# Kernel tuning notes

Hardware: AMD Instinct MI355X
Metric: run time of the kernel (lower is better)

The kernel has to match this reference:

```python
import jax, jax.numpy as jnp
import numpy as np

B, T, D = 4, 2048, 768
H = 12
DH = D // H
DFF = 3072
EPS = 1e-5


def _layernorm(x, g, b):
    mu = jnp.mean(x, axis=-1, keepdims=True)
    var = jnp.var(x, axis=-1, keepdims=True)
    return (x - mu) * jax.lax.rsqrt(var + EPS) * g + b


def setup_inputs() -> dict:
    key = jax.random.key(0)
    ks = jax.random.split(key, 12)
    s = lambda fan_in: 1.0 / np.sqrt(fan_in)
    return {
        "x": jax.random.normal(ks[0], (B, T, D), dtype=jnp.float32),
        "ln1_g": jnp.ones((D,), jnp.float32),
        "ln1_b": jnp.zeros((D,), jnp.float32),
        "w_qkv": jax.random.uniform(ks[1], (D, 3 * D), jnp.float32, -s(D), s(D)),
        "b_qkv": jax.random.uniform(ks[2], (3 * D,), jnp.float32, -s(D), s(D)),
        "w_proj": jax.random.uniform(ks[3], (D, D), jnp.float32, -s(D), s(D)),
        "b_proj": jax.random.uniform(ks[4], (D,), jnp.float32, -s(D), s(D)),
        "ln2_g": jnp.ones((D,), jnp.float32),
        "ln2_b": jnp.zeros((D,), jnp.float32),
        "w_ff1": jax.random.uniform(ks[5], (D, DFF), jnp.float32, -s(D), s(D)),
        "b_ff1": jax.random.uniform(ks[6], (DFF,), jnp.float32, -s(D), s(D)),
        "w_ff2": jax.random.uniform(ks[7], (DFF, D), jnp.float32, -s(DFF), s(DFF)),
        "b_ff2": jax.random.uniform(ks[8], (D,), jnp.float32, -s(DFF), s(DFF)),
    }


def reference(x, ln1_g, ln1_b, w_qkv, b_qkv, w_proj, b_proj,
              ln2_g, ln2_b, w_ff1, b_ff1, w_ff2, b_ff2):
    # --- attention sublayer ---
    h = _layernorm(x, ln1_g, ln1_b)
    qkv = h @ w_qkv + b_qkv                       # [B,T,3D]
    q, k, v = jnp.split(qkv, 3, axis=-1)
    q = q.reshape(B, T, H, DH).transpose(0, 2, 1, 3)  # [B,H,T,DH]
    k = k.reshape(B, T, H, DH).transpose(0, 2, 1, 3)
    v = v.reshape(B, T, H, DH).transpose(0, 2, 1, 3)
    att = jnp.einsum('bhqd,bhkd->bhqk', q, k) / jnp.sqrt(jnp.float32(DH))
    causal = jnp.tril(jnp.ones((T, T), dtype=bool))
    att = jnp.where(causal, att, -jnp.inf)
    att = jax.nn.softmax(att, axis=-1)
    out = jnp.einsum('bhqk,bhkd->bhqd', att, v)    # [B,H,T,DH]
    out = out.transpose(0, 2, 1, 3).reshape(B, T, D)
    x = x + out @ w_proj + b_proj
    # --- MLP sublayer ---
    h2 = _layernorm(x, ln2_g, ln2_b)
    h2 = jax.nn.gelu(h2 @ w_ff1 + b_ff1, approximate=False)
    x = x + h2 @ w_ff2 + b_ff2
    return x
```

## Files before the change

### kernel.cpp

```cpp
#include <hip/hip_runtime.h>
#include <cstdint>
#include <cstddef>

typedef unsigned short u16;
typedef unsigned int u32;
typedef __attribute__((ext_vector_type(8))) short s16x8;
typedef __attribute__((ext_vector_type(4))) float f32x4;

#define NB 4
#define NT 2048
#define ND 768
#define NH 12
#define NDH 64
#define NFF 3072
#define NM (NB*NT)

__device__ __forceinline__ u16 f2b(float f){
  union { float f; unsigned u; } c; c.f = f;
  unsigned r = c.u + 0x7fffu + ((c.u >> 16) & 1u);
  return (u16)(r >> 16);
}

__device__ __forceinline__ f32x4 mfma16(s16x8 a, s16x8 b, f32x4 c){
  return __builtin_amdgcn_mfma_f32_16x16x32_bf16(a, b, c, 0, 0, 0);
}

__device__ __forceinline__ void stage16(u16* lds, const u16* g){
  __builtin_amdgcn_global_load_lds(
      (const __attribute__((address_space(1))) unsigned int*)g,
      (__attribute__((address_space(3))) unsigned int*)lds,
      16, 0, 0);
}

__global__ __launch_bounds__(256) void transpose_bf16(
    const float* __restrict__ in, u16* __restrict__ out, int K, int N)
{
  __shared__ float tile[32][33];
  const int n0 = blockIdx.x * 32, k0 = blockIdx.y * 32;
  const int tx = threadIdx.x, ty = threadIdx.y;
  #pragma unroll
  for (int i = 0; i < 32; i += 8)
    tile[ty + i][tx] = in[(size_t)(k0 + ty + i) * N + n0 + tx];
  __syncthreads();
  #pragma unroll
  for (int i = 0; i < 32; i += 8)
    out[(size_t)(n0 + ty + i) * K + k0 + tx] = f2b(tile[tx][ty + i]);
}

__global__ __launch_bounds__(256) void ln_kernel(
    const float* __restrict__ x, const float* __restrict__ g,
    const float* __restrict__ b, u16* __restrict__ out)
{
  const int row = blockIdx.x;
  const int t = threadIdx.x;
  const float* xr = x + (size_t)row * ND;
  float v0 = xr[t], v1 = xr[t + 256], v2 = xr[t + 512];
  float s = v0 + v1 + v2;
  float ss = v0*v0 + v1*v1 + v2*v2;
  #pragma unroll
  for (int o = 32; o; o >>= 1) { s += __shfl_xor(s, o, 64); ss += __shfl_xor(ss, o, 64); }
  __shared__ float red[8];
  const int w = t >> 6;
  if ((t & 63) == 0) { red[w] = s; red[4 + w] = ss; }
  __syncthreads();
  s  = red[0] + red[1] + red[2] + red[3];
  ss = red[4] + red[5] + red[6] + red[7];
  const float mu = s * (1.f / ND);
  const float var = ss * (1.f / ND) - mu * mu;
  const float rinv = rsqrtf(var + 1e-5f);
  u16* orow = out + (size_t)row * ND;
  orow[t]       = f2b((v0 - mu) * rinv * g[t]       + b[t]);
  orow[t + 256] = f2b((v1 - mu) * rinv * g[t + 256] + b[t + 256]);
  orow[t + 512] = f2b((v2 - mu) * rinv * g[t + 512] + b[t + 512]);
}

template<int EPI>
__global__ __launch_bounds__(256,4) void gemm_bt(
    const u16* __restrict__ A, const u16* __restrict__ Bt,
    const float* __restrict__ bias, const float* __restrict__ res,
    void* __restrict__ o0, void* __restrict__ o1, void* __restrict__ o2,
    const int M, const int N, const int K)
{
  __shared__ u16 As[2][128 * 32];
  __shared__ u16 Bs[2][128 * 32];
  const int tid = threadIdx.x;
  const int lane = tid & 63, wid = tid >> 6;
  const int wr = wid >> 1, wc = wid & 1;
  const int lg = lane >> 4, lm = lane & 15;
  const int bm = blockIdx.x * 128, bn = blockIdx.y * 128;

  f32x4 acc[4][4] = {};

  const u16* ApT = A  + (size_t)(bm + (tid >> 2)) * K + (tid & 3) * 8;
  const u16* BpT = Bt + (size_t)(bn + (tid >> 2)) * K + (tid & 3) * 8;
  const size_t rs64 = (size_t)64 * K;
  const int woff = wid * 512;

  stage16(&As[0][woff],        ApT);
  stage16(&As[0][woff + 2048], ApT + rs64);
  stage16(&Bs[0][woff],        BpT);
  stage16(&Bs[0][woff + 2048], BpT + rs64);
  __syncthreads();

  int cur = 0;
  const int nt = K >> 5;
  for (int t = 1; t < nt; ++t) {
    const int k0 = t << 5;
    stage16(&As[cur ^ 1][woff],        ApT + k0);
    stage16(&As[cur ^ 1][woff + 2048], ApT + rs64 + k0);
    stage16(&Bs[cur ^ 1][woff],        BpT + k0);
    stage16(&Bs[cur ^ 1][woff + 2048], BpT + rs64 + k0);
    s16x8 af[4], bf[4];
    #pragma unroll
    for (int i = 0; i < 4; i++) af[i] = *(const s16x8*)&As[cur][(wr * 64 + i * 16 + lm) * 32 + lg * 8];
    #pragma unroll
    for (int j = 0; j < 4; j++) bf[j] = *(const s16x8*)&Bs[cur][(wc * 64 + j * 16 + lm) * 32 + lg * 8];
    #pragma unroll
    for (int i = 0; i < 4; i++)
      #pragma unroll
      for (int j = 0; j < 4; j++)
        acc[i][j] = mfma16(af[i], bf[j], acc[i][j]);
    __syncthreads();
    cur ^= 1;
  }
  {
    s16x8 af[4], bf[4];
    #pragma unroll
    for (int i = 0; i < 4; i++) af[i] = *(const s16x8*)&As[cur][(wr * 64 + i * 16 + lm) * 32 + lg * 8];
    #pragma unroll
    for (int j = 0; j < 4; j++) bf[j] = *(const s16x8*)&Bs[cur][(wc * 64 + j * 16 + lm) * 32 + lg * 8];
    #pragma unroll
    for (int i = 0; i < 4; i++)
      #pragma unroll
      for (int j = 0; j < 4; j++)
        acc[i][j] = mfma16(af[i], bf[j], acc[i][j]);
  }

  #pragma unroll
  for (int i = 0; i < 4; i++)
    #pragma unroll
    for (int j = 0; j < 4; j++) {
      const int col = bn + wc * 64 + j * 16 + lm;
      const float bb = bias[col];
      #pragma unroll
      for (int r = 0; r < 4; r++) {
        const int row = bm + wr * 64 + i * 16 + lg * 4 + r;
        float v = acc[i][j][r] + bb;
        if (EPI == 0) {
          u16* dst; int rem;
          if (col < ND)            { dst = (u16*)o0; rem = col; v *= 0.125f; }
          else if (col < 2 * ND)   { dst = (u16*)o1; rem = col - ND; }
          else                     { dst = (u16*)o2; rem = col - 2 * ND; }
          const int hh = rem >> 6, dh = rem & 63;
          const int bb2 = row >> 11, tt = row & 2047;
          dst[(((size_t)bb2 * NH + hh) * NT + tt) * NDH + dh] = f2b(v);
        } else if (EPI == 1) {
          ((float*)o0)[(size_t)row * ND + col] = v + res[(size_t)row * ND + col];
        } else if (EPI == 2) {
          const float ge = 0.5f * v * (1.f + erff(v * 0.70710678118654752f));
          ((u16*)o0)[(size_t)row * NFF + col] = f2b(ge);
        } else {
          ((float*)o0)[(size_t)row * ND + col] = v + res[(size_t)row * ND + col];
        }
      }
    }
}

__global__ __launch_bounds__(256,2) void attn_kernel(
    const u16* __restrict__ Q, const u16* __restrict__ Kg,
    const u16* __restrict__ V, u16* __restrict__ O)
{
  const int pairIdx = blockIdx.x;
  const int bh = blockIdx.y;
  const int b = bh / NH, h = bh % NH;
  const int tid = threadIdx.x;
  const int lane = tid & 63, w = tid >> 6;
  const int lg = lane >> 4, lm = lane & 15;
  const int sr = tid >> 3;
  const int sc = (tid & 7) * 8;

  __shared__ u16 Ks[64 * 64];
  __shared__ u16 Vt[64 * 64];
  __shared__ u16 Ps[4][16 * 64];

  const u16* Qb = Q  + (size_t)bh * NT * NDH;
  const u16* Kb = Kg + (size_t)bh * NT * NDH;
  const u16* Vb = V  + (size_t)bh * NT * NDH;

  for (int half = 0; half < 2; ++half) {
    const int si = half ? (31 - pairIdx) : pairIdx;
    const int q0 = si * 64;
    const int ktmax = si;

    const s16x8 qf0 = *(const s16x8*)&Qb[(size_t)(q0 + w * 16 + lm) * NDH + lg * 8];
    const s16x8 qf1 = *(const s16x8*)&Qb[(size_t)(q0 + w * 16 + lm) * NDH + 32 + lg * 8];

    f32x4 oacc[4] = {};
    float m = -INFINITY, l = 0.f;

    s16x8 kva = *(const s16x8*)&Kb[(size_t)sr * NDH + sc];
    s16x8 kvb = *(const s16x8*)&Kb[(size_t)(sr + 32) * NDH + sc];
    s16x8 vva = *(const s16x8*)&Vb[(size_t)sr * NDH + sc];
    s16x8 vvb = *(const s16x8*)&Vb[(size_t)(sr + 32) * NDH + sc];

    for (int kt = 0; kt <= ktmax; ++kt) {
      __syncthreads();
      *(s16x8*)&Ks[sr * 64 + (sc ^ ((sr & 7) << 3))] = kva;
      *(s16x8*)&Ks[(sr + 32) * 64 + (sc ^ ((sr & 7) << 3))] = kvb;
      #pragma unroll
      for (int e = 0; e < 8; ++e)
        Vt[(sc + e) * 64 + (sr ^ ((tid & 7) << 3))] = (u16)vva[e];
      #pragma unroll
      for (int e = 0; e < 8; ++e)
        Vt[(sc + e) * 64 + ((sr + 32) ^ ((tid & 7) << 3))] = (u16)vvb[e];
      __syncthreads();

      if (kt < ktmax) {
        const u16* Kn = Kb + (size_t)(kt + 1) * 64 * NDH;
        const u16* Vn = Vb + (size_t)(kt + 1) * 64 * NDH;
        kva = *(const s16x8*)&Kn[(size_t)sr * NDH + sc];
        kvb = *(const s16x8*)&Kn[(size_t)(sr + 32) * NDH + sc];
        vva = *(const s16x8*)&Vn[(size_t)sr * NDH + sc];
        vvb = *(const s16x8*)&Vn[(size_t)(sr + 32) * NDH + sc];
      }

      f32x4 sv[4];
      #pragma unroll
      for (int n = 0; n < 4; ++n) {
        const int krow = (n * 16 + lm) * 64;
        const int swz = (lm & 7) << 3;
        s16x8 kf0 = *(const s16x8*)&Ks[krow + ((lg * 8) ^ swz)];
        s16x8 kf1 = *(const s16x8*)&Ks[krow + ((32 + lg * 8) ^ swz)];
        f32x4 s4 = {};
        s4 = mfma16(kf0, qf0, s4);
        s4 = mfma16(kf1, qf1, s4);
        sv[n] = s4;
      }

      if (kt == ktmax) {
        #pragma unroll
        for (int n = 0; n < 4; ++n)
          #pragma unroll
          for (int r = 0; r < 4; ++r)
            if (n * 16 + lg * 4 + r > w * 16 + lm) sv[n][r] = -INFINITY;
      }

      float mx = -INFINITY;
      #pragma unroll
      for (int n = 0; n < 4; ++n)
        #pragma unroll
        for (int r = 0; r < 4; ++r) mx = fmaxf(mx, sv[n][r]);
      mx = fmaxf(mx, __shfl_xor(mx, 16));
      mx = fmaxf(mx, __shfl_xor(mx, 32));
      const float mnew = fmaxf(m, mx);
      const float alpha = __expf(m - mnew);
      m = mnew;

      float rs = 0.f;
      u32 pk[4][2];
      #pragma unroll
      for (int n = 0; n < 4; ++n) {
        const float p0 = __expf(sv[n][0] - mnew);
        const float p1 = __expf(sv[n][1] - mnew);
        const float p2 = __expf(sv[n][2] - mnew);
        const float p3 = __expf(sv[n][3] - mnew);
        rs += (p0 + p1) + (p2 + p3);
        pk[n][0] = (u32)f2b(p0) | ((u32)f2b(p1) << 16);
        pk[n][1] = (u32)f2b(p2) | ((u32)f2b(p3) << 16);
      }
      rs += __shfl_xor(rs, 16);
      rs += __shfl_xor(rs, 32);
      l = l * alpha + rs;

      #pragma unroll
      for (int n = 0; n < 4; ++n) {
        const int idx0 = lm * 64 + ((n * 16 + lg * 4) ^ ((lm & 7) << 3));
        *(u32*)&Ps[w][idx0] = pk[n][0];
        *(u32*)&Ps[w][idx0 + 2] = pk[n][1];
      }

      float av[4];
      #pragma unroll
      for (int r = 0; r < 4; ++r) av[r] = __shfl(alpha, lg * 4 + r);
      #pragma unroll
      for (int d = 0; d < 4; ++d)
        #pragma unroll
        for (int r = 0; r < 4; ++r) oacc[d][r] *= av[r];

      #pragma unroll
      for (int kh = 0; kh < 2; ++kh) {
        const s16x8 pf = *(const s16x8*)&Ps[w][lm * 64 + ((kh * 32 + lg * 8) ^ ((lm & 7) << 3))];
        #pragma unroll
        for (int dt = 0; dt < 4; ++dt) {
          const int g = (2 * dt + (lm >> 3)) & 7;
          const s16x8 vf = *(const s16x8*)&Vt[(dt * 16 + lm) * 64 + (((kh * 4 + lg) ^ g) << 3)];
          oacc[dt] = mfma16(pf, vf, oacc[dt]);
        }
      }
    }

    float lv[4];
    #pragma unroll
    for (int r = 0; r < 4; ++r) lv[r] = 1.f / __shfl(l, lg * 4 + r);
    #pragma unroll
    for (int dt = 0; dt < 4; ++dt)
      #pragma unroll
      for (int r = 0; r < 4; ++r) {
        const int qg = q0 + w * 16 + lg * 4 + r;
        O[((size_t)b * NT + qg) * ND + h * NDH + dt * 16 + lm] = f2b(oacc[dt][r] * lv[r]);
      }
  }
}

extern "C" void kernel_launch(void* const* d_in, const int* in_sizes, int n_in,
                              void* d_out, int out_size, void* d_ws, size_t ws_size,
                              hipStream_t stream)
{
  const float* x      = (const float*)d_in[0];
  const float* ln1_g  = (const float*)d_in[1];
  const float* ln1_b  = (const float*)d_in[2];
  const float* w_qkv  = (const float*)d_in[3];
  const float* b_qkv  = (const float*)d_in[4];
  const float* w_proj = (const float*)d_in[5];
  const float* b_proj = (const float*)d_in[6];
  const float* ln2_g  = (const float*)d_in[7];
  const float* ln2_b  = (const float*)d_in[8];
  const float* w_ff1  = (const float*)d_in[9];
  const float* b_ff1  = (const float*)d_in[10];
  const float* w_ff2  = (const float*)d_in[11];
  const float* b_ff2  = (const float*)d_in[12];

  char* ws = (char*)d_ws;
  u16*   wt_qkv = (u16*)(ws + 0);
  u16*   wt_proj= (u16*)(ws + 3538944);
  u16*   wt_ff1 = (u16*)(ws + 4718592);
  u16*   wt_ff2 = (u16*)(ws + 9437184);
  u16*   hbuf   = (u16*)(ws + 14155776);
  u16*   qbuf   = (u16*)(ws + 26738688);
  u16*   kbuf   = (u16*)(ws + 39321600);
  u16*   vbuf   = (u16*)(ws + 51904512);
  u16*   aobuf  = (u16*)(ws + 64487424);
  float* x1     = (float*)(ws + 77070336);
  u16*   h2buf  = (u16*)(ws + 102236160);
  u16*   ff1buf = hbuf;

  transpose_bf16<<<dim3(2304/32,  768/32), dim3(32,8), 0, stream>>>(w_qkv,  wt_qkv,  768, 2304);
  transpose_bf16<<<dim3( 768/32,  768/32), dim3(32,8), 0, stream>>>(w_proj, wt_proj, 768,  768);
  transpose_bf16<<<dim3(3072/32,  768/32), dim3(32,8), 0, stream>>>(w_ff1,  wt_ff1,  768, 3072);
  transpose_bf16<<<dim3( 768/32, 3072/32), dim3(32,8), 0, stream>>>(w_ff2,  wt_ff2, 3072,  768);

  ln_kernel<<<NM, 256, 0, stream>>>(x, ln1_g, ln1_b, hbuf);
  gemm_bt<0><<<dim3(NM/128, 2304/128), 256, 0, stream>>>(hbuf, wt_qkv, b_qkv, nullptr,
                                                         qbuf, kbuf, vbuf, NM, 2304, ND);
  attn_kernel<<<dim3(16, NB*NH), 256, 0, stream>>>(qbuf, kbuf, vbuf, aobuf);
  gemm_bt<1><<<dim3(NM/128, ND/128), 256, 0, stream>>>(aobuf, wt_proj, b_proj, x,
                                                       x1, nullptr, nullptr, NM, ND, ND);
  ln_kernel<<<NM, 256, 0, stream>>>(x1, ln2_g, ln2_b, h2buf);
  gemm_bt<2><<<dim3(NM/128, NFF/128), 256, 0, stream>>>(h2buf, wt_ff1, b_ff1, nullptr,
                                                        ff1buf, nullptr, nullptr, NM, NFF, ND);
  gemm_bt<3><<<dim3(NM/128, ND/128), 256, 0, stream>>>(ff1buf, wt_ff2, b_ff2, x1,
                                                       d_out, nullptr, nullptr, NM, ND, NFF);
}
```

Measured before the change: 306.8 us.

## Triple-buffer GEMM LDS staging with vmcnt waits and XOR-swizzled layout

Replaces the double-buffered K loop in the bf16 GEMM with a three-stage LDS ring. Loads are issued two tiles ahead, and explicit s_waitcnt vmcnt plus a raw barrier replace the per-iteration __syncthreads. It also XOR-swizzles the 16-byte chunk position within each LDS row on both the store and fragment-read side to reduce bank conflicts. LDS use grows to 48KB per block, so launch bounds drop to 3 blocks per CU, which reduces occupancy. Correctness depends on stage16 being an asynchronous direct-to-LDS load counted by vmcnt.

New measurement: 302.5 us. No clear change (-1.4%).

```diff
diff --git a/kernel.cpp b/kernel.cpp
--- a/kernel.cpp
+++ b/kernel.cpp
@@ -75,14 +75,14 @@
 }
 
 template<int EPI>
-__global__ __launch_bounds__(256,4) void gemm_bt(
+__global__ __launch_bounds__(256,3) void gemm_bt(
     const u16* __restrict__ A, const u16* __restrict__ Bt,
     const float* __restrict__ bias, const float* __restrict__ res,
     void* __restrict__ o0, void* __restrict__ o1, void* __restrict__ o2,
     const int M, const int N, const int K)
 {
-  __shared__ u16 As[2][128 * 32];
-  __shared__ u16 Bs[2][128 * 32];
+  __shared__ u16 As[3][128 * 32];
+  __shared__ u16 Bs[3][128 * 32];
   const int tid = threadIdx.x;
   const int lane = tid & 63, wid = tid >> 6;
   const int wr = wid >> 1, wc = wid & 1;
@@ -91,44 +91,47 @@
 
   f32x4 acc[4][4] = {};
 
-  const u16* ApT = A  + (size_t)(bm + (tid >> 2)) * K + (tid & 3) * 8;
-  const u16* BpT = Bt + (size_t)(bn + (tid >> 2)) * K + (tid & 3) * 8;
+  const int srow = tid >> 2;
+  const int schunk = (tid & 3) ^ ((tid >> 3) & 3);
+  const u16* ApT = A  + (size_t)(bm + srow) * K + schunk * 8;
+  const u16* BpT = Bt + (size_t)(bn + srow) * K + schunk * 8;
   const size_t rs64 = (size_t)64 * K;
   const int woff = wid * 512;
+  const int fswz = (lm >> 1) & 3;
+
+  const int nt = K >> 5;
 
   stage16(&As[0][woff],        ApT);
   stage16(&As[0][woff + 2048], ApT + rs64);
   stage16(&Bs[0][woff],        BpT);
   stage16(&Bs[0][woff + 2048], BpT + rs64);
-  __syncthreads();
-
-  int cur = 0;
-  const int nt = K >> 5;
-  for (int t = 1; t < nt; ++t) {
-    const int k0 = t << 5;
-    stage16(&As[cur ^ 1][woff],        ApT + k0);
-    stage16(&As[cur ^ 1][woff + 2048], ApT + rs64 + k0);
-    stage16(&Bs[cur ^ 1][woff],        BpT + k0);
-    stage16(&Bs[cur ^ 1][woff + 2048], BpT + rs64 + k0);
+  stage16(&As[1][woff],        ApT + 32);
+  stage16(&As[1][woff + 2048], ApT + rs64 + 32);
+  stage16(&Bs[1][woff],        BpT + 32);
+  stage16(&Bs[1][woff + 2048], BpT + rs64 + 32);
+
+  for (int t = 0; t < nt; ++t) {
+    if (t < nt - 1) asm volatile("s_waitcnt vmcnt(4)" ::: "memory");
+    else            asm volatile("s_waitcnt vmcnt(0)" ::: "memory");
+    __builtin_amdgcn_s_barrier();
+    __builtin_amdgcn_sched_barrier(0);
+    if (t + 2 < nt) {
+      const int k0 = (t + 2) << 5;
+      const int wb = (t + 2) % 3;
+      stage16(&As[wb][woff],        ApT + k0);
+      stage16(&As[wb][woff + 2048], ApT + rs64 + k0);
+      stage16(&Bs[wb][woff],        BpT + k0);
+      stage16(&Bs[wb][woff + 2048], BpT + rs64 + k0);
+    }
+    __builtin_amdgcn_sched_barrier(0);
+    const int rb = t % 3;
     s16x8 af[4], bf[4];
     #pragma unroll
-    for (int i = 0; i < 4; i++) af[i] = *(const s16x8*)&As[cur][(wr * 64 + i * 16 + lm) * 32 + lg * 8];
-    #pragma unroll
-    for (int j = 0; j < 4; j++) bf[j] = *(const s16x8*)&Bs[cur][(wc * 64 + j * 16 + lm) * 32 + lg * 8];
-    #pragma unroll
     for (int i = 0; i < 4; i++)
-      #pragma unroll
-      for (int j = 0; j < 4; j++)
-        acc[i][j] = mfma16(af[i], bf[j], acc[i][j]);
-    __syncthreads();
-    cur ^= 1;
-  }
-  {
-    s16x8 af[4], bf[4];
-    #pragma unroll
-    for (int i = 0; i < 4; i++) af[i] = *(const s16x8*)&As[cur][(wr * 64 + i * 16 + lm) * 32 + lg * 8];
-    #pragma unroll
-    for (int j = 0; j < 4; j++) bf[j] = *(const s16x8*)&Bs[cur][(wc * 64 + j * 16 + lm) * 32 + lg * 8];
+      af[i] = *(const s16x8*)&As[rb][(wr * 64 + i * 16 + lm) * 32 + ((lg ^ fswz) * 8)];
+    #pragma unroll
+    for (int j = 0; j < 4; j++)
+      bf[j] = *(const s16x8*)&Bs[rb][(wc * 64 + j * 16 + lm) * 32 + ((lg ^ fswz) * 8)];
     #pragma unroll
     for (int i = 0; i < 4; i++)
       #pragma unroll
```
